# Kernel tuning notes

Measured on AMD Instinct MI355X. Metric: run time of the kernel, lower is better.

## Reference

```python
import jax, jax.numpy as jnp
import numpy as np

B, L, D = 64, 512, 128  # batch, word_len, dim


def setup_inputs() -> dict:
    key = jax.random.key(0)
    ks = jax.random.split(key, 12)
    p = lambda k, s: jax.random.normal(k, s, dtype=jnp.float32) * 0.05
    return {
        "EW": jax.random.normal(ks[0], (B, L, D), dtype=jnp.float32),
        "ES": jax.random.normal(ks[1], (B, L, D), dtype=jnp.float32),
        "WQ_w": p(ks[2], (D, D)), "WQ_b": p(ks[3], (D,)),
        "WK_w": p(ks[4], (D, D)), "WK_b": p(ks[5], (D,)),
        "UQ_w": p(ks[6], (D, D)), "UQ_b": p(ks[7], (D,)),
        "UK_w": p(ks[8], (D, D)), "UK_b": p(ks[9], (D,)),
        "V_w": p(ks[10], (D, D)), "V_b": p(ks[11], (D,)),
    }


def reference(EW, ES, WQ_w, WQ_b, WK_w, WK_b, UQ_w, UQ_b, UK_w, UK_b, V_w, V_b):
    dim = EW.shape[-1]
    word_len = EW.shape[-2]
    scale = 1.0 / (2.0 * dim ** 0.5)
    # word-level Q/K and sentence-level UQ/UK projections (torch Linear: x @ W.T + b)
    Q = (EW @ WQ_w.T + WQ_b) * scale   # [B, L, D]
    K = (EW @ WK_w.T + WK_b) * scale   # [B, L, D]
    UQ = (ES @ UQ_w.T + UQ_b) * scale  # [B, L, D]
    UK = (ES @ UK_w.T + UK_b) * scale  # [B, L, D]
    # two-term score matrix [B, L, L]
    alpha = jnp.einsum('bid,bjd->bij', Q, K) + jnp.einsum('bid,bjd->bij', UQ, UK)
    # manual exp/sum softmax exactly as in the source (no max subtraction;
    # denominator is broadcast along axis 1, faithful to unsqueeze(1))
    numerator = jnp.exp(alpha)                      # [B, L, L]
    denominator = numerator.sum(axis=-1)[:, None, :]  # [B, 1, L]
    soft = numerator / denominator                  # [B, L, L]
    value = EW @ V_w.T + V_b                        # [B, L, D]
    # faithful reinterpreting view (NOT a transpose): [B, L, D] -> [B, D, L]
    value = value.reshape(-1, dim, word_len)
    result = value @ soft                           # [B, D, L]
    return result.reshape(-1, word_len, dim)        # [B, L, D]
```

## Files before the change

kernel.cpp:

```cpp
#include <hip/hip_runtime.h>
#include <hip/hip_bf16.h>

#define NB 64
#define NL 512
#define ND 128
#define NK 256

typedef unsigned short ush;
typedef __attribute__((ext_vector_type(8))) short short8;
typedef __attribute__((ext_vector_type(16))) float f32x16;


__device__ __forceinline__ ush f2bs(float f) {
    union { __hip_bfloat16 h; ush u; } cv;
    cv.h = __float2bfloat16(f);
    return cv.u;
}
__device__ __forceinline__ short8 pack_bf8(float4 a, float4 b) {
    short8 r;
    r[0] = (short)f2bs(a.x); r[1] = (short)f2bs(a.y);
    r[2] = (short)f2bs(a.z); r[3] = (short)f2bs(a.w);
    r[4] = (short)f2bs(b.x); r[5] = (short)f2bs(b.y);
    r[6] = (short)f2bs(b.z); r[7] = (short)f2bs(b.w);
    return r;
}
__device__ __forceinline__ f32x16 zero16() {
    f32x16 z = {0.f,0.f,0.f,0.f,0.f,0.f,0.f,0.f,0.f,0.f,0.f,0.f,0.f,0.f,0.f,0.f};
    return z;
}

__global__ __launch_bounds__(256) void wconv_kernel(
    const float* __restrict__ W0, const float* __restrict__ W1,
    const float* __restrict__ W2, const float* __restrict__ W3,
    const float* __restrict__ W4, ush* __restrict__ Wb)
{
    const int m = blockIdx.y;
    const float* W = (m == 0) ? W0 : (m == 1) ? W1 : (m == 2) ? W2 : (m == 3) ? W3 : W4;
    const int e = (blockIdx.x * 256 + threadIdx.x) * 4;
    float4 v = *(const float4*)(W + e);
    ushort4 o;
    o.x = f2bs(v.x); o.y = f2bs(v.y); o.z = f2bs(v.z); o.w = f2bs(v.w);
    *(ushort4*)(Wb + m * 16384 + e) = o;
}

__global__ __launch_bounds__(256) void projqk_kernel(
    const float* __restrict__ EW, const float* __restrict__ ES,
    const ush* __restrict__ Wb,
    const float* __restrict__ b0, const float* __restrict__ b1,
    const float* __restrict__ b2, const float* __restrict__ b3,
    ush* __restrict__ QUf, ush* __restrict__ KUf)
{
    __shared__ ush Tls[4][2048];
    const int f = blockIdx.x;
    const int xcd = f & 7, loc = f >> 3;
    const int rt = xcd * 32 + (loc >> 2);
    const int m  = loc & 3;
    const int tid = threadIdx.x, w = tid >> 6, lane = tid & 63;
    const int l5 = lane & 31, hi = lane >> 5;
    const float* X = (m >= 2) ? ES : EW;
    const int rbase = rt * 128 + w * 32;

    const float* xr = X + (size_t)(rbase + l5) * ND + hi * 8;
    short8 af[8];
    #pragma unroll
    for (int ks = 0; ks < 8; ++ks)
        af[ks] = pack_bf8(*(const float4*)(xr + ks * 16),
                          *(const float4*)(xr + ks * 16 + 4));

    const ush* Wm = Wb + m * 16384;
    const float* Bp = (m == 0) ? b0 : (m == 1) ? b1 : (m == 2) ? b2 : b3;
    const float scl = 0.044194173824159216f;

    f32x16 acc[4];
    acc[0] = zero16(); acc[1] = zero16(); acc[2] = zero16(); acc[3] = zero16();
    #pragma unroll
    for (int ks = 0; ks < 8; ++ks) {
        #pragma unroll
        for (int nb = 0; nb < 4; ++nb) {
            short8 bf_ = *(const short8*)(Wm + (nb * 32 + l5) * 128 + ks * 16 + hi * 8);
            acc[nb] = __builtin_amdgcn_mfma_f32_32x32x16_bf16(af[ks], bf_, acc[nb], 0, 0, 0);
        }
    }

    char* Tc = (char*)Tls[w];
    ush* dstf = (m == 0 || m == 2) ? QUf : KUf;
    const int ko = (m >= 2) ? 8 : 0;
    const int p_g = rt * 4 + w;
    #pragma unroll
    for (int pass = 0; pass < 2; ++pass) {
        #pragma unroll
        for (int nbl = 0; nbl < 2; ++nbl) {
            const int nb = pass * 2 + nbl;
            float bias = Bp[nb * 32 + l5];
            #pragma unroll
            for (int r6 = 0; r6 < 16; ++r6) {
                int row = (r6 & 3) + 8 * (r6 >> 2) + 4 * hi;
                int boff = row * 128 + (((nbl * 32 + l5) * 2) ^ ((row & 7) << 4));
                *(ush*)(Tc + boff) = f2bs((acc[nb][r6] + bias) * scl);
            }
        }
        #pragma unroll
        for (int ks8 = 0; ks8 < 4; ++ks8) {
            int boff = l5 * 128 + ((ks8 * 32 + hi * 16) ^ ((l5 & 7) << 4));
            short8 v = *(const short8*)(Tc + boff);
            int ksg = ko + pass * 4 + ks8;
            *(short8*)(dstf + ((size_t)(p_g * 16 + ksg) * 64 + lane) * 8) = v;
        }
    }
}

__global__ __launch_bounds__(256) void projv_kernel(
    const float* __restrict__ EW, const ush* __restrict__ Wb,
    const float* __restrict__ b4, ush* __restrict__ Vbf)
{
    __shared__ ush lds[16384];
    const int f = blockIdx.x;
    const int rt = (f & 7) * 32 + (f >> 3);
    const int tid = threadIdx.x, w = tid >> 6, lane = tid & 63;
    const int l5 = lane & 31, hi = lane >> 5;
    const int rbase = rt * 128 + w * 32;

    const float* xr = EW + (size_t)(rbase + l5) * ND + hi * 8;
    short8 af[8];
    #pragma unroll
    for (int ks = 0; ks < 8; ++ks)
        af[ks] = pack_bf8(*(const float4*)(xr + ks * 16),
                          *(const float4*)(xr + ks * 16 + 4));

    const ush* Wm = Wb + 4 * 16384;
    f32x16 acc[4];
    acc[0] = zero16(); acc[1] = zero16(); acc[2] = zero16(); acc[3] = zero16();
    #pragma unroll
    for (int ks = 0; ks < 8; ++ks) {
        #pragma unroll
        for (int nb = 0; nb < 4; ++nb) {
            short8 bf_ = *(const short8*)(Wm + (nb * 32 + l5) * 128 + ks * 16 + hi * 8);
            acc[nb] = __builtin_amdgcn_mfma_f32_32x32x16_bf16(af[ks], bf_, acc[nb], 0, 0, 0);
        }
    }

    char* Lc = (char*)lds;
    #pragma unroll
    for (int nb = 0; nb < 4; ++nb) {
        float bias = b4[nb * 32 + l5];
        #pragma unroll
        for (int r6 = 0; r6 < 16; ++r6) {
            int row5 = (r6 & 3) + 8 * (r6 >> 2) + 4 * hi;
            int dl = w * 8 + (row5 >> 2);
            int lcol = (row5 & 3) * 128 + nb * 32 + l5;
            int boff = dl * 1024 + ((lcol * 2) ^ ((dl & 7) << 4));
            *(ush*)(Lc + boff) = f2bs(acc[nb][r6] + bias);
        }
    }
    __syncthreads();
    #pragma unroll
    for (int it = 0; it < 8; ++it) {
        int chunk = it * 256 + tid;
        int ks = chunk >> 6, ln = chunk & 63;
        int l5b = ln & 31, hib = ln >> 5;
        int boff = l5b * 1024 + ((ks * 32 + hib * 16) ^ ((l5b & 7) << 4));
        short8 v = *(const short8*)(Lc + boff);
        *(short8*)(Vbf + ((size_t)(rt * 32 + ks) * 64 + ln) * 8) = v;
    }
}

__global__ __launch_bounds__(256) void alpha_kernel(
    const ush* __restrict__ QUf, const ush* __restrict__ KUf,
    ush* __restrict__ Nf, float* __restrict__ denomInv)
{
    __shared__ float red[4][2][16];
    __shared__ ush TlsA[4][2048];
    const int f = blockIdx.x;
    const int xcd = f & 7, loc = f >> 3;
    const int b  = xcd * 8 + (loc >> 4);
    const int rt = loc & 15;
    const int tid = threadIdx.x, w = tid >> 6, lane = tid & 63;
    const int l5 = lane & 31, hi = lane >> 5;
    const ush* Qb = QUf + (size_t)b * 131072;
    const ush* Kb = KUf + (size_t)b * 131072;
    ush* Nfb = Nf + (size_t)b * 262144;

    short8 aq[16];
    const ush* qp = Qb + (size_t)rt * 8192 + lane * 8;
    #pragma unroll
    for (int ks = 0; ks < 16; ++ks) aq[ks] = *(const short8*)(qp + ks * 512);

    f32x16 acc[4];
    acc[0] = zero16(); acc[1] = zero16(); acc[2] = zero16(); acc[3] = zero16();
    #pragma unroll 2
    for (int ks = 0; ks < 16; ++ks) {
        #pragma unroll
        for (int cp = 0; cp < 4; ++cp) {
            const ush* kp = Kb + (size_t)((w * 4 + cp) * 16 + ks) * 512 + lane * 8;
            acc[cp] = __builtin_amdgcn_mfma_f32_32x32x16_bf16(aq[ks], *(const short8*)kp,
                                                              acc[cp], 0, 0, 0);
        }
    }

    float rs[16];
    #pragma unroll
    for (int r6 = 0; r6 < 16; ++r6) rs[r6] = 0.f;
    char* Tc = (char*)TlsA[w];
    #pragma unroll
    for (int cp = 0; cp < 4; ++cp) {
        const int cpg = w * 4 + cp;
        float e[16];
        #pragma unroll
        for (int r6 = 0; r6 < 16; ++r6) { e[r6] = __expf(acc[cp][r6]); rs[r6] += e[r6]; }
        #pragma unroll
        for (int q = 0; q < 8; ++q) {
            int r6 = q * 2;
            int r = (r6 & 3) + 8 * (r6 >> 2) + 4 * hi;
            unsigned int pk = (unsigned int)f2bs(e[r6])
                            | ((unsigned int)f2bs(e[r6 + 1]) << 16);
            *(unsigned int*)(Tc + l5 * 128 + ((r * 2) ^ ((l5 & 7) << 4))) = pk;
        }
        #pragma unroll
        for (int ksl = 0; ksl < 2; ++ksl) {
            short8 v = *(const short8*)(Tc + l5 * 128 +
                           (((ksl * 16 + hi * 8) * 2) ^ ((l5 & 7) << 4)));
            int ksg = rt * 2 + ksl;
            *(short8*)(Nfb + ((size_t)(cpg * 32 + ksg) * 64 + lane) * 8) = v;
        }
    }

    #pragma unroll
    for (int mk = 1; mk <= 16; mk <<= 1)
        #pragma unroll
        for (int r6 = 0; r6 < 16; ++r6) rs[r6] += __shfl_xor(rs[r6], mk, 32);
    if (l5 == 0)
        #pragma unroll
        for (int r6 = 0; r6 < 16; ++r6) red[w][hi][r6] = rs[r6];
    __syncthreads();
    if (tid < 32) {
        int t = tid;
        int hh = (t >> 2) & 1, r6 = (t & 3) + 4 * (t >> 3);
        float s = red[0][hh][r6] + red[1][hh][r6] + red[2][hh][r6] + red[3][hh][r6];
        denomInv[b * NL + rt * 32 + t] = 1.0f / s;
    }
}

__global__ __launch_bounds__(256) void pv_kernel(
    const ush* __restrict__ Vbf, const ush* __restrict__ Nf,
    const float* __restrict__ denomInv, float* __restrict__ out)
{
    const int f = blockIdx.x;
    const int xcd = f & 7, loc = f >> 3;
    const int b  = xcd * 8 + (loc >> 3);
    const int ct = loc & 7;
    const int tid = threadIdx.x, w = tid >> 6, lane = tid & 63;
    const int l5 = lane & 31, hi = lane >> 5;
    const ush* Vbb = Vbf + (size_t)b * 65536;
    const ush* Nfb = Nf + (size_t)b * 262144;
    const size_t obase = (size_t)b * (ND * NL);

    const ush* vp  = Vbb + (size_t)w * 16384 + lane * 8;
    const ush* np0 = Nfb + (size_t)(ct * 2) * 16384 + lane * 8;
    const ush* np1 = np0 + 16384;

    f32x16 acc0 = zero16(), acc1 = zero16();
    #pragma unroll 2
    for (int ks = 0; ks < 32; ++ks) {
        short8 va = *(const short8*)(vp + ks * 512);
        acc0 = __builtin_amdgcn_mfma_f32_32x32x16_bf16(va, *(const short8*)(np0 + ks * 512), acc0, 0, 0, 0);
        acc1 = __builtin_amdgcn_mfma_f32_32x32x16_bf16(va, *(const short8*)(np1 + ks * 512), acc1, 0, 0, 0);
    }
    const int c0 = ct * 64;
    float rd0 = denomInv[b * NL + c0 + l5];
    float rd1 = denomInv[b * NL + c0 + 32 + l5];
    #pragma unroll
    for (int r6 = 0; r6 < 16; ++r6) {
        int d = w * 32 + (r6 & 3) + 8 * (r6 >> 2) + 4 * hi;
        out[obase + (size_t)d * NL + c0 + l5]      = acc0[r6] * rd0;
        out[obase + (size_t)d * NL + c0 + 32 + l5] = acc1[r6] * rd1;
    }
}

__global__ __launch_bounds__(256) void fused_kernel(
    const ush* __restrict__ QUf, const ush* __restrict__ KUf,
    const ush* __restrict__ Vbf, float* __restrict__ out)
{
    __shared__ ush Pt[32 * 136];
    __shared__ float red[128];
    __shared__ float rdenS[32];
    const int f = blockIdx.x;
    const int xcd = f & 7, loc = f >> 3;
    const int b  = xcd * 8 + (loc >> 4);
    const int ct = loc & 15, c0 = ct * 32;
    const int tid = threadIdx.x, w = tid >> 6, lane = tid & 63;
    const int l5 = lane & 31, hi = lane >> 5;
    const ush* Qb  = QUf + (size_t)b * 131072;
    const ush* Kb  = KUf + (size_t)b * 131072;
    const ush* Vbb = Vbf + (size_t)b * 65536;
    const size_t obase = (size_t)b * (ND * NL);

    {
        short8 aq[16];
        const ush* qp = Qb + (size_t)ct * 8192 + lane * 8;
        #pragma unroll
        for (int ks = 0; ks < 16; ++ks) aq[ks] = *(const short8*)(qp + ks * 512);
        float rs[16];
        #pragma unroll
        for (int r = 0; r < 16; ++r) rs[r] = 0.f;
        #pragma unroll
        for (int t = 0; t < 4; ++t) {
            const ush* kp = Kb + (size_t)(w * 4 + t) * 8192 + lane * 8;
            f32x16 a0 = zero16(), a1 = zero16();
            #pragma unroll
            for (int ks = 0; ks < 16; ks += 2) {
                a0 = __builtin_amdgcn_mfma_f32_32x32x16_bf16(aq[ks],     *(const short8*)(kp + ks * 512),       a0, 0, 0, 0);
                a1 = __builtin_amdgcn_mfma_f32_32x32x16_bf16(aq[ks + 1], *(const short8*)(kp + (ks + 1) * 512), a1, 0, 0, 0);
            }
            #pragma unroll
            for (int r = 0; r < 16; ++r) rs[r] += __expf(a0[r] + a1[r]);
        }
        #pragma unroll
        for (int mk = 1; mk <= 16; mk <<= 1)
            #pragma unroll
            for (int r = 0; r < 16; ++r) rs[r] += __shfl_xor(rs[r], mk, 32);
        if (l5 == 0)
            #pragma unroll
            for (int r = 0; r < 16; ++r) red[(w * 2 + hi) * 16 + r] = rs[r];
    }
    __syncthreads();
    if (tid < 32) {
        int c = tid;
        int h2 = (c >> 2) & 1, r = (c & 3) + 4 * (c >> 3);
        float s = 0.f;
        #pragma unroll
        for (int kh = 0; kh < 4; ++kh) s += red[(kh * 2 + h2) * 16 + r];
        rdenS[c] = 1.0f / s;
    }
    __syncthreads();

    const int p2 = w;
    const float rden = rdenS[l5];
    const ush* kp2 = Kb + (size_t)ct * 8192 + lane * 8;
    f32x16 oA = zero16(), oB = zero16();

    for (int it = 0; it < 4; ++it) {
        if (it) __syncthreads();
        const ush* qp2 = Qb + (size_t)(it * 4 + p2) * 8192 + lane * 8;
        f32x16 s0 = zero16(), s1 = zero16();
        #pragma unroll
        for (int ks = 0; ks < 16; ks += 2) {
            s0 = __builtin_amdgcn_mfma_f32_32x32x16_bf16(*(const short8*)(qp2 + ks * 512),
                                                         *(const short8*)(kp2 + ks * 512),       s0, 0, 0, 0);
            s1 = __builtin_amdgcn_mfma_f32_32x32x16_bf16(*(const short8*)(qp2 + (ks + 1) * 512),
                                                         *(const short8*)(kp2 + (ks + 1) * 512), s1, 0, 0, 0);
        }
        #pragma unroll
        for (int q = 0; q < 4; ++q) {
            ushort4 pv;
            pv.x = f2bs(__expf(s0[q * 4 + 0] + s1[q * 4 + 0]) * rden);
            pv.y = f2bs(__expf(s0[q * 4 + 1] + s1[q * 4 + 1]) * rden);
            pv.z = f2bs(__expf(s0[q * 4 + 2] + s1[q * 4 + 2]) * rden);
            pv.w = f2bs(__expf(s0[q * 4 + 3] + s1[q * 4 + 3]) * rden);
            int boff = l5 * 272 + (((p2 * 32 + q * 8 + hi * 4) * 2) ^ ((l5 & 7) << 4));
            *(ushort4*)((char*)Pt + boff) = pv;
        }
        __syncthreads();
        #pragma unroll
        for (int j = 0; j < 8; j += 2) {
            short8 va0 = *(const short8*)(Vbb + ((size_t)(p2 * 32 + it * 8 + j) * 64 + lane) * 8);
            short8 pb0 = *(const short8*)((char*)Pt + l5 * 272 + (((j * 16 + hi * 8) * 2) ^ ((l5 & 7) << 4)));
            oA = __builtin_amdgcn_mfma_f32_32x32x16_bf16(va0, pb0, oA, 0, 0, 0);
            short8 va1 = *(const short8*)(Vbb + ((size_t)(p2 * 32 + it * 8 + j + 1) * 64 + lane) * 8);
            short8 pb1 = *(const short8*)((char*)Pt + l5 * 272 + ((((j + 1) * 16 + hi * 8) * 2) ^ ((l5 & 7) << 4)));
            oB = __builtin_amdgcn_mfma_f32_32x32x16_bf16(va1, pb1, oB, 0, 0, 0);
        }
    }
    f32x16 oacc = oA + oB;
    #pragma unroll
    for (int r = 0; r < 16; ++r) {
        int d = p2 * 32 + (r & 3) + 8 * (r >> 2) + 4 * hi;
        out[obase + (size_t)d * NL + c0 + l5] = oacc[r];
    }
}

extern "C" void kernel_launch(void* const* d_in, const int* in_sizes, int n_in,
                              void* d_out, int out_size, void* d_ws, size_t ws_size,
                              hipStream_t stream)
{
    const float* EW   = (const float*)d_in[0];
    const float* ES   = (const float*)d_in[1];
    const float* WQ_w = (const float*)d_in[2];
    const float* WQ_b = (const float*)d_in[3];
    const float* WK_w = (const float*)d_in[4];
    const float* WK_b = (const float*)d_in[5];
    const float* UQ_w = (const float*)d_in[6];
    const float* UQ_b = (const float*)d_in[7];
    const float* UK_w = (const float*)d_in[8];
    const float* UK_b = (const float*)d_in[9];
    const float* V_w  = (const float*)d_in[10];
    const float* V_b  = (const float*)d_in[11];

    if (ws_size < (size_t)41 * 1024 * 1024) return;

    char* ws = (char*)d_ws;
    ush* QUf = (ush*)ws;
    ush* KUf = (ush*)(ws + (size_t)16 * 1024 * 1024);
    ush* Vbf = (ush*)(ws + (size_t)32 * 1024 * 1024);
    ush* Wb  = (ush*)(ws + (size_t)40 * 1024 * 1024);
    float* dInv = (float*)(ws + (size_t)40 * 1024 * 1024 + 512 * 1024);
    ush* Nf  = (ush*)(ws + (size_t)41 * 1024 * 1024);
    float* outp = (float*)d_out;

    wconv_kernel<<<dim3(16, 5), 256, 0, stream>>>(WQ_w, WK_w, UQ_w, UK_w, V_w, Wb);
    projqk_kernel<<<1024, 256, 0, stream>>>(EW, ES, Wb,
                                            WQ_b, WK_b, UQ_b, UK_b, QUf, KUf);
    projv_kernel<<<256, 256, 0, stream>>>(EW, Wb, V_b, Vbf);
    if (ws_size >= (size_t)74 * 1024 * 1024) {
        alpha_kernel<<<1024, 256, 0, stream>>>(QUf, KUf, Nf, dInv);
        pv_kernel<<<512, 256, 0, stream>>>(Vbf, Nf, dInv, outp);
    } else {
        fused_kernel<<<1024, 256, 0, stream>>>(QUf, KUf, Vbf, outp);
    }
}
```

Before: 93.11 us.

## Split alpha and PV kernels into more blocks with partial denominators

The alpha kernel now splits each row tile's column range in two, so it launches twice as many blocks. Each block writes a partial row sum instead of the inverse denominator, and the Q fragments are loaded per k-step rather than held as 16 registers. The PV kernel covers 32 columns per block instead of 64, again doubling the grid, and uses two accumulators over alternating k-steps that are summed at the end. The aim is better occupancy and latency hiding through lower register pressure and more parallel blocks. The cost is that Q and V are re-read by more blocks, and PV has to sum the two partials and take the reciprocal itself.

```diff
diff --git a/kernel.cpp b/kernel.cpp
--- a/kernel.cpp
+++ b/kernel.cpp
@@ -166,34 +166,37 @@
 
 __global__ __launch_bounds__(256) void alpha_kernel(
     const ush* __restrict__ QUf, const ush* __restrict__ KUf,
-    ush* __restrict__ Nf, float* __restrict__ denomInv)
+    ush* __restrict__ Nf, float* __restrict__ dPart)
 {
     __shared__ float red[4][2][16];
     __shared__ ush TlsA[4][2048];
     const int f = blockIdx.x;
     const int xcd = f & 7, loc = f >> 3;
-    const int b  = xcd * 8 + (loc >> 4);
-    const int rt = loc & 15;
+    const int b  = xcd * 8 + (loc >> 5);
+    const int rt = (loc >> 1) & 15;
+    const int ch = loc & 1;
     const int tid = threadIdx.x, w = tid >> 6, lane = tid & 63;
     const int l5 = lane & 31, hi = lane >> 5;
     const ush* Qb = QUf + (size_t)b * 131072;
     const ush* Kb = KUf + (size_t)b * 131072;
     ush* Nfb = Nf + (size_t)b * 262144;
 
-    short8 aq[16];
     const ush* qp = Qb + (size_t)rt * 8192 + lane * 8;
-    #pragma unroll
-    for (int ks = 0; ks < 16; ++ks) aq[ks] = *(const short8*)(qp + ks * 512);
-
-    f32x16 acc[4];
-    acc[0] = zero16(); acc[1] = zero16(); acc[2] = zero16(); acc[3] = zero16();
-    #pragma unroll 2
-    for (int ks = 0; ks < 16; ++ks) {
-        #pragma unroll
-        for (int cp = 0; cp < 4; ++cp) {
-            const ush* kp = Kb + (size_t)((w * 4 + cp) * 16 + ks) * 512 + lane * 8;
-            acc[cp] = __builtin_amdgcn_mfma_f32_32x32x16_bf16(aq[ks], *(const short8*)kp,
-                                                              acc[cp], 0, 0, 0);
+    const int cpg0 = ch * 8 + w * 2;
+
+    f32x16 a0[2], a1[2];
+    a0[0] = zero16(); a0[1] = zero16(); a1[0] = zero16(); a1[1] = zero16();
+    #pragma unroll
+    for (int ks = 0; ks < 16; ks += 2) {
+        short8 aqa = *(const short8*)(qp + ks * 512);
+        short8 aqb = *(const short8*)(qp + (ks + 1) * 512);
+        #pragma unroll
+        for (int cp = 0; cp < 2; ++cp) {
+            const ush* kp = Kb + (size_t)((cpg0 + cp) * 16) * 512 + lane * 8;
+            a0[cp] = __builtin_amdgcn_mfma_f32_32x32x16_bf16(aqa,
+                         *(const short8*)(kp + ks * 512), a0[cp], 0, 0, 0);
+            a1[cp] = __builtin_amdgcn_mfma_f32_32x32x16_bf16(aqb,
+                         *(const short8*)(kp + (ks + 1) * 512), a1[cp], 0, 0, 0);
         }
     }
 
@@ -202,11 +205,14 @@
     for (int r6 = 0; r6 < 16; ++r6) rs[r6] = 0.f;
     char* Tc = (char*)TlsA[w];
     #pragma unroll
-    for (int cp = 0; cp < 4; ++cp) {
-        const int cpg = w * 4 + cp;
+    for (int cp = 0; cp < 2; ++cp) {
+        const int cpg = cpg0 + cp;
         float e[16];
         #pragma unroll
-        for (int r6 = 0; r6 < 16; ++r6) { e[r6] = __expf(acc[cp][r6]); rs[r6] += e[r6]; }
+        for (int r6 = 0; r6 < 16; ++r6) {
+            e[r6] = __expf(a0[cp][r6] + a1[cp][r6]);
+            rs[r6] += e[r6];
+        }
         #pragma unroll
         for (int q = 0; q < 8; ++q) {
             int r6 = q * 2;
@@ -236,43 +242,43 @@
         int t = tid;
         int hh = (t >> 2) & 1, r6 = (t & 3) + 4 * (t >> 3);
         float s = red[0][hh][r6] + red[1][hh][r6] + red[2][hh][r6] + red[3][hh][r6];
-        denomInv[b * NL + rt * 32 + t] = 1.0f / s;
+        dPart[((size_t)b * 2 + ch) * NL + rt * 32 + t] = s;
     }
 }
 
 __global__ __launch_bounds__(256) void pv_kernel(
     const ush* __restrict__ Vbf, const ush* __restrict__ Nf,
-    const float* __restrict__ denomInv, float* __restrict__ out)
+    const float* __restrict__ dPart, float* __restrict__ out)
 {
     const int f = blockIdx.x;
     const int xcd = f & 7, loc = f >> 3;
-    const int b  = xcd * 8 + (loc >> 3);
-    const int ct = loc & 7;
+    const int b  = xcd * 8 + (loc >> 4);
+    const int ct = loc & 15;
     const int tid = threadIdx.x, w = tid >> 6, lane = tid & 63;
     const int l5 = lane & 31, hi = lane >> 5;
     const ush* Vbb = Vbf + (size_t)b * 65536;
     const ush* Nfb = Nf + (size_t)b * 262144;
     const size_t obase = (size_t)b * (ND * NL);
 
-    const ush* vp  = Vbb + (size_t)w * 16384 + lane * 8;
-    const ush* np0 = Nfb + (size_t)(ct * 2) * 16384 + lane * 8;
-    const ush* np1 = np0 + 16384;
+    const ush* vp = Vbb + (size_t)w * 16384 + lane * 8;
+    const ush* np = Nfb + (size_t)ct * 16384 + lane * 8;
 
     f32x16 acc0 = zero16(), acc1 = zero16();
-    #pragma unroll 2
-    for (int ks = 0; ks < 32; ++ks) {
-        short8 va = *(const short8*)(vp + ks * 512);
-        acc0 = __builtin_amdgcn_mfma_f32_32x32x16_bf16(va, *(const short8*)(np0 + ks * 512), acc0, 0, 0, 0);
-        acc1 = __builtin_amdgcn_mfma_f32_32x32x16_bf16(va, *(const short8*)(np1 + ks * 512), acc1, 0, 0, 0);
-    }
-    const int c0 = ct * 64;
-    float rd0 = denomInv[b * NL + c0 + l5];
-    float rd1 = denomInv[b * NL + c0 + 32 + l5];
+    #pragma unroll
+    for (int ks = 0; ks < 32; ks += 2) {
+        acc0 = __builtin_amdgcn_mfma_f32_32x32x16_bf16(*(const short8*)(vp + ks * 512),
+                   *(const short8*)(np + ks * 512), acc0, 0, 0, 0);
+        acc1 = __builtin_amdgcn_mfma_f32_32x32x16_bf16(*(const short8*)(vp + (ks + 1) * 512),
+                   *(const short8*)(np + (ks + 1) * 512), acc1, 0, 0, 0);
+    }
+    f32x16 acc = acc0 + acc1;
+    const int c0 = ct * 32;
+    float rd = 1.0f / (dPart[((size_t)b * 2 + 0) * NL + c0 + l5]
+                     + dPart[((size_t)b * 2 + 1) * NL + c0 + l5]);
     #pragma unroll
     for (int r6 = 0; r6 < 16; ++r6) {
         int d = w * 32 + (r6 & 3) + 8 * (r6 >> 2) + 4 * hi;
-        out[obase + (size_t)d * NL + c0 + l5]      = acc0[r6] * rd0;
-        out[obase + (size_t)d * NL + c0 + 32 + l5] = acc1[r6] * rd1;
+        out[obase + (size_t)d * NL + c0 + l5] = acc[r6] * rd;
     }
 }
 
@@ -402,7 +408,7 @@
     ush* KUf = (ush*)(ws + (size_t)16 * 1024 * 1024);
     ush* Vbf = (ush*)(ws + (size_t)32 * 1024 * 1024);
     ush* Wb  = (ush*)(ws + (size_t)40 * 1024 * 1024);
-    float* dInv = (float*)(ws + (size_t)40 * 1024 * 1024 + 512 * 1024);
+    float* dPart = (float*)(ws + (size_t)40 * 1024 * 1024 + 512 * 1024);
     ush* Nf  = (ush*)(ws + (size_t)41 * 1024 * 1024);
     float* outp = (float*)d_out;
 
@@ -411,8 +417,8 @@
                                             WQ_b, WK_b, UQ_b, UK_b, QUf, KUf);
     projv_kernel<<<256, 256, 0, stream>>>(EW, Wb, V_b, Vbf);
     if (ws_size >= (size_t)74 * 1024 * 1024) {
-        alpha_kernel<<<1024, 256, 0, stream>>>(QUf, KUf, Nf, dInv);
-        pv_kernel<<<512, 256, 0, stream>>>(Vbf, Nf, dInv, outp);
+        alpha_kernel<<<2048, 256, 0, stream>>>(QUf, KUf, Nf, dPart);
+        pv_kernel<<<1024, 256, 0, stream>>>(Vbf, Nf, dPart, outp);
     } else {
         fused_kernel<<<1024, 256, 0, stream>>>(QUf, KUf, Vbf, outp);
     }
```

Result: faster. 80.86 us (-13.2%).
